# Optimization experiments

Hardware: AMD Instinct MI355X
Metric: run time of the kernel (lower is better)

Reference implementation:

```python
import jax, jax.numpy as jnp
import numpy as np

N_NODES = 100000
N_EDGES = 1600000
IN_FEATS, HID, NUM_CLS = 128, 128, 40


def setup_inputs() -> dict:
    key = jax.random.key(0)
    ks = jax.random.split(key, 5)
    x = jax.random.normal(ks[0], (N_NODES, IN_FEATS), dtype=jnp.float32)
    # xavier-like scale for weights
    W1 = jax.random.normal(ks[1], (IN_FEATS, HID), dtype=jnp.float32) * (1.0 / np.sqrt(IN_FEATS))
    b1 = jnp.zeros((HID,), dtype=jnp.float32)
    W2 = jax.random.normal(ks[2], (HID, NUM_CLS), dtype=jnp.float32) * (1.0 / np.sqrt(HID))
    b2 = jnp.zeros((NUM_CLS,), dtype=jnp.float32)
    src = jax.random.randint(ks[3], (N_EDGES,), 0, N_NODES, dtype=jnp.int32)
    dst = jax.random.randint(ks[4], (N_EDGES,), 0, N_NODES, dtype=jnp.int32)
    return {"x": x, "W1": W1, "b1": b1, "W2": W2, "b2": b2, "src": src, "dst": dst}


def _graph_conv(h, W, b, src, dst, src_norm, dst_norm, n_nodes):
    # DGL GraphConv, norm='both': D_out^{-1/2} A D_in^{-1/2} H W + b
    # (weight-first vs aggregate-first ordering in DGL is mathematically identical)
    hs = h * src_norm[:, None]                      # [N, d] source-side norm
    msg = hs[src]                                   # [E, d] gather
    agg = jax.ops.segment_sum(msg, dst, num_segments=n_nodes)  # [N, d] scatter-add
    agg = agg * dst_norm[:, None]                   # dest-side norm
    return agg @ W + b


def reference(x, W1, b1, W2, b2, src, dst):
    n = x.shape[0]
    ones = jnp.ones(src.shape[0], dtype=x.dtype)
    out_deg = jnp.clip(jax.ops.segment_sum(ones, src, num_segments=n), 1.0)
    in_deg = jnp.clip(jax.ops.segment_sum(ones, dst, num_segments=n), 1.0)
    src_norm = out_deg ** -0.5
    dst_norm = in_deg ** -0.5
    h = jax.nn.relu(_graph_conv(x, W1, b1, src, dst, src_norm, dst_norm, n))
    return _graph_conv(h, W2, b2, src, dst, src_norm, dst_norm, n)
```

## Files before the change

### kernel.cpp

```cpp
#include <hip/hip_runtime.h>

constexpr int NN   = 100000;
constexpr int NE   = 1600000;
constexpr int INF  = 128;
constexpr int NC   = 40;

constexpr int BKSH = 9;
constexpr int NBK  = (NN + 511) / 512;
constexpr int EPB  = 4096;
constexpr int PBLK = (NE + EPB - 1) / EPB;
constexpr int CAP  = 14336;
constexpr int HB   = 391;

typedef __attribute__((ext_vector_type(8))) short short8;
typedef __attribute__((ext_vector_type(4))) float f32x4;

__device__ __forceinline__ float bflo(unsigned int u) { return __uint_as_float(u << 16); }
__device__ __forceinline__ float bfhi(unsigned int u) { return __uint_as_float(u & 0xffff0000u); }
__device__ __forceinline__ unsigned short f2bf(float f) {
    unsigned int u = __float_as_uint(f);
    return (unsigned short)((u + 0x7fffu + ((u >> 16) & 1u)) >> 16);
}
__device__ __forceinline__ unsigned int pack2(float a, float b) {
    return (unsigned int)f2bf(a) | ((unsigned int)f2bf(b) << 16);
}

__global__ __launch_bounds__(256) void histconv_kernel(const int* __restrict__ src,
                                                       const int* __restrict__ dst,
                                                       unsigned int* __restrict__ bcntD,
                                                       unsigned int* __restrict__ bcntS,
                                                       const float* __restrict__ x,
                                                       const float* __restrict__ W1,
                                                       const float* __restrict__ W2,
                                                       unsigned short* __restrict__ xh,
                                                       unsigned short* __restrict__ w1t,
                                                       unsigned short* __restrict__ w2t) {
    const int b = blockIdx.x;
    const int tid = threadIdx.x;
    if (b < HB) {
        __shared__ unsigned int hcD[NBK];
        __shared__ unsigned int hcS[NBK];
        for (int i = tid; i < NBK; i += 256) { hcD[i] = 0u; hcS[i] = 0u; }
        __syncthreads();
        int gid = b * 256 + tid;
        int stride = HB * 256;
        for (int e = gid; e < NE; e += stride) {
            atomicAdd(&hcD[dst[e] >> BKSH], 1u);
            atomicAdd(&hcS[src[e] >> BKSH], 1u);
        }
        __syncthreads();
        for (int i = tid; i < NBK; i += 256) {
            if (hcD[i]) atomicAdd(&bcntD[i], hcD[i]);
            if (hcS[i]) atomicAdd(&bcntS[i], hcS[i]);
        }
    } else if (b < HB + 6250) {
        int j = (b - HB) * 256 + tid;
        float4 v0 = ((const float4*)x)[2 * j];
        float4 v1 = ((const float4*)x)[2 * j + 1];
        uint4 o;
        o.x = pack2(v0.x, v0.y);
        o.y = pack2(v0.z, v0.w);
        o.z = pack2(v1.x, v1.y);
        o.w = pack2(v1.z, v1.w);
        ((uint4*)xh)[j] = o;
    } else if (b == HB + 6250) {
        for (int i = tid; i < 128 * 128; i += 256) {
            int k = i >> 7, n = i & 127;
            w1t[n * 128 + k] = f2bf(W1[i]);
        }
    } else {
        for (int i = tid; i < 48 * 128; i += 256) {
            int n = i >> 7, k = i & 127;
            w2t[i] = f2bf((n < NC) ? W2[k * NC + n] : 0.f);
        }
    }
}

__global__ __launch_bounds__(256) void partition_kernel(const int* __restrict__ src,
                                                        const int* __restrict__ dst,
                                                        const unsigned int* __restrict__ bcntD,
                                                        const unsigned int* __restrict__ bcntS,
                                                        int* __restrict__ curD_g,
                                                        int* __restrict__ curS_g,
                                                        int* __restrict__ epartsD,
                                                        unsigned short* __restrict__ epartsS) {
    __shared__ int sc[256];
    __shared__ int cntD[NBK], gadjD[NBK], curD[NBK];
    __shared__ int cntS[NBK], gadjS[NBK], curS[NBK];
    __shared__ int baselD[NBK], baselS[NBK];
    __shared__ int stageD[EPB];
    __shared__ unsigned short stageS[EPB];
    __shared__ unsigned char bidD[EPB];
    __shared__ unsigned char bidS[EPB];
    const int tid = threadIdx.x;
    const int e0 = blockIdx.x * EPB;
    const int total = min(EPB, NE - e0);

    {
        int v = (tid < NBK) ? (int)bcntD[tid] : 0;
        sc[tid] = v;
        __syncthreads();
        for (int off = 1; off < 256; off <<= 1) {
            int t = (tid >= off) ? sc[tid - off] : 0;
            __syncthreads();
            sc[tid] += t;
            __syncthreads();
        }
        if (tid < NBK) baselD[tid] = sc[tid] - v;
        __syncthreads();
        v = (tid < NBK) ? (int)bcntS[tid] : 0;
        sc[tid] = v;
        __syncthreads();
        for (int off = 1; off < 256; off <<= 1) {
            int t = (tid >= off) ? sc[tid - off] : 0;
            __syncthreads();
            sc[tid] += t;
            __syncthreads();
        }
        if (tid < NBK) baselS[tid] = sc[tid] - v;
    }
    for (int i = tid; i < NBK; i += 256) { cntD[i] = 0; cntS[i] = 0; }
    __syncthreads();
    for (int i = tid; i < total; i += 256) {
        atomicAdd(&cntD[dst[e0 + i] >> BKSH], 1);
        atomicAdd(&cntS[src[e0 + i] >> BKSH], 1);
    }
    __syncthreads();
    {
        int v = (tid < NBK) ? cntD[tid] : 0;
        sc[tid] = v;
        __syncthreads();
        for (int off = 1; off < 256; off <<= 1) {
            int t = (tid >= off) ? sc[tid - off] : 0;
            __syncthreads();
            sc[tid] += t;
            __syncthreads();
        }
        if (tid < NBK) {
            int excl = sc[tid] - v;
            curD[tid] = excl;
            int g = (v > 0) ? atomicAdd(&curD_g[tid], v) : 0;
            gadjD[tid] = baselD[tid] + g - excl;
        }
        __syncthreads();
        v = (tid < NBK) ? cntS[tid] : 0;
        sc[tid] = v;
        __syncthreads();
        for (int off = 1; off < 256; off <<= 1) {
            int t = (tid >= off) ? sc[tid - off] : 0;
            __syncthreads();
            sc[tid] += t;
            __syncthreads();
        }
        if (tid < NBK) {
            int excl = sc[tid] - v;
            curS[tid] = excl;
            int g = (v > 0) ? atomicAdd(&curS_g[tid], v) : 0;
            gadjS[tid] = baselS[tid] + g - excl;
        }
    }
    __syncthreads();
    for (int i = tid; i < total; i += 256) {
        int s = src[e0 + i];
        int d = dst[e0 + i];
        int bD = d >> BKSH;
        int offD = atomicAdd(&curD[bD], 1);
        stageD[offD] = s | ((d - (bD << BKSH)) << 17);
        bidD[offD] = (unsigned char)bD;
        int bS = s >> BKSH;
        int offS = atomicAdd(&curS[bS], 1);
        stageS[offS] = (unsigned short)(s - (bS << BKSH));
        bidS[offS] = (unsigned char)bS;
    }
    __syncthreads();
    for (int j = tid; j < total; j += 256) {
        int b = bidD[j];
        epartsD[gadjD[b] + j] = stageD[j];
    }
    for (int j = tid; j < total; j += 256) {
        int b = bidS[j];
        epartsS[gadjS[b] + j] = stageS[j];
    }
}

__global__ __launch_bounds__(512) void pass2_kernel(const int* __restrict__ epartsD,
                                                    const unsigned short* __restrict__ epartsS,
                                                    const unsigned int* __restrict__ bcntD,
                                                    const unsigned int* __restrict__ bcntS,
                                                    int* __restrict__ row_ptr,
                                                    int* __restrict__ esrc,
                                                    float* __restrict__ srcn,
                                                    float* __restrict__ dstn) {
    __shared__ int hist[512];
    __shared__ int cur[512];
    __shared__ int histS[512];
    __shared__ int lesrc[CAP];
    __shared__ int base_s, cnt_s, baseS_s, cntS_s;
    const int tid = threadIdx.x;
    const int b = blockIdx.x;

    {
        int v = (tid < NBK) ? (int)bcntD[tid] : 0;
        hist[tid] = v;
        __syncthreads();
        for (int off = 1; off < 512; off <<= 1) {
            int t = (tid >= off) ? hist[tid - off] : 0;
            __syncthreads();
            hist[tid] += t;
            __syncthreads();
        }
        if (tid == b) { base_s = hist[b] - v; cnt_s = v; }
        __syncthreads();
        v = (tid < NBK) ? (int)bcntS[tid] : 0;
        hist[tid] = v;
        __syncthreads();
        for (int off = 1; off < 512; off <<= 1) {
            int t = (tid >= off) ? hist[tid - off] : 0;
            __syncthreads();
            hist[tid] += t;
            __syncthreads();
        }
        if (tid == b) { baseS_s = hist[b] - v; cntS_s = v; }
        __syncthreads();
    }
    const int base = base_s;
    const int cnt = cnt_s;
    const int baseS = baseS_s;
    const int cntS = cntS_s;
    const int n0 = b << BKSH;
    const int nloc = min(512, NN - n0);

    hist[tid] = 0;
    histS[tid] = 0;
    __syncthreads();
    for (int j = tid; j < cnt; j += 512)
        atomicAdd(&hist[epartsD[base + j] >> 17], 1);
    for (int j = tid; j < cntS; j += 512)
        atomicAdd(&histS[(int)epartsS[baseS + j]], 1);
    __syncthreads();
    int myc = hist[tid];
    int mycS = histS[tid];
    for (int off = 1; off < 512; off <<= 1) {
        int t = (tid >= off) ? hist[tid - off] : 0;
        __syncthreads();
        hist[tid] += t;
        __syncthreads();
    }
    int excl = hist[tid] - myc;
    cur[tid] = excl;
    if (tid < nloc) {
        int g = n0 + tid;
        row_ptr[g] = base + excl;
        dstn[g] = rsqrtf(fmaxf((float)myc, 1.0f));
        srcn[g] = rsqrtf(fmaxf((float)mycS, 1.0f));
    }
    if (b == NBK - 1 && tid == 0) row_ptr[NN] = NE;
    __syncthreads();
    if (cnt <= CAP) {
        for (int j = tid; j < cnt; j += 512) {
            int rec = epartsD[base + j];
            int pos = atomicAdd(&cur[rec >> 17], 1);
            lesrc[pos] = rec & 0x1FFFF;
        }
        __syncthreads();
        for (int j = tid; j < cnt; j += 512) esrc[base + j] = lesrc[j];
    } else {
        for (int j = tid; j < cnt; j += 512) {
            int rec = epartsD[base + j];
            int pos = atomicAdd(&cur[rec >> 17], 1);
            esrc[base + pos] = rec & 0x1FFFF;
        }
    }
}

__global__ __launch_bounds__(256) void gather1_kernel(const int* __restrict__ row_ptr,
                                                      const int* __restrict__ esrc,
                                                      const unsigned short* __restrict__ xh,
                                                      const float* __restrict__ src_norm,
                                                      unsigned short* __restrict__ aggb) {
    int node = (blockIdx.x * blockDim.x + threadIdx.x) >> 6;
    int lane = threadIdx.x & 63;
    if (node >= NN) return;
    int beg = __builtin_amdgcn_readfirstlane(row_ptr[node]);
    int end = __builtin_amdgcn_readfirstlane(row_ptr[node + 1]);
    const int quad = lane >> 4;
    const int l16  = lane & 15;
    float acc0 = 0.f, acc1 = 0.f, acc2 = 0.f, acc3 = 0.f;
    float acc4 = 0.f, acc5 = 0.f, acc6 = 0.f, acc7 = 0.f;
    for (int e = beg; e < end; e += 16) {
        const int rem = end - e;
        int s[4];
#pragma unroll
        for (int t = 0; t < 4; ++t) {
            int slot = t * 4 + quad;
            int idx = (slot < rem) ? (e + slot) : beg;
            s[t] = esrc[idx];
        }
        float n[4];
        uint4 u[4];
#pragma unroll
        for (int t = 0; t < 4; ++t) {
            int slot = t * 4 + quad;
            n[t] = (slot < rem) ? src_norm[s[t]] : 0.f;
            u[t] = ((const uint4*)(xh + (size_t)s[t] * INF))[l16];
        }
#pragma unroll
        for (int t = 0; t < 4; ++t) {
            acc0 += bflo(u[t].x) * n[t];
            acc1 += bfhi(u[t].x) * n[t];
            acc2 += bflo(u[t].y) * n[t];
            acc3 += bfhi(u[t].y) * n[t];
            acc4 += bflo(u[t].z) * n[t];
            acc5 += bfhi(u[t].z) * n[t];
            acc6 += bflo(u[t].w) * n[t];
            acc7 += bfhi(u[t].w) * n[t];
        }
    }
    acc0 += __shfl_down(acc0, 32); acc1 += __shfl_down(acc1, 32);
    acc2 += __shfl_down(acc2, 32); acc3 += __shfl_down(acc3, 32);
    acc4 += __shfl_down(acc4, 32); acc5 += __shfl_down(acc5, 32);
    acc6 += __shfl_down(acc6, 32); acc7 += __shfl_down(acc7, 32);
    acc0 += __shfl_down(acc0, 16); acc1 += __shfl_down(acc1, 16);
    acc2 += __shfl_down(acc2, 16); acc3 += __shfl_down(acc3, 16);
    acc4 += __shfl_down(acc4, 16); acc5 += __shfl_down(acc5, 16);
    acc6 += __shfl_down(acc6, 16); acc7 += __shfl_down(acc7, 16);
    if (lane < 16) {
        uint4 o;
        o.x = pack2(acc0, acc1);
        o.y = pack2(acc2, acc3);
        o.z = pack2(acc4, acc5);
        o.w = pack2(acc6, acc7);
        ((uint4*)(aggb + (size_t)node * INF))[l16] = o;
    }
}

__global__ __launch_bounds__(256) void gemm12_kernel(const unsigned short* __restrict__ aggb,
                                                     const unsigned short* __restrict__ w1t,
                                                     const unsigned short* __restrict__ w2t,
                                                     const float* __restrict__ b1,
                                                     const float* __restrict__ dstn,
                                                     const float* __restrict__ srcn,
                                                     unsigned short* __restrict__ hwb) {
    __shared__ unsigned short At[64 * 128];
    __shared__ unsigned short W1l[128 * 128];
    __shared__ unsigned short W2l[48 * 128];
    __shared__ float dn[64], sn[64], b1l[128];
    const int tid = threadIdx.x;
    const int r0 = blockIdx.x * 64;

    {
        const uint4* g1 = (const uint4*)w1t;
        uint4* s1 = (uint4*)W1l;
        for (int i = tid; i < 2048; i += 256) s1[i] = g1[i];
        const uint4* g2 = (const uint4*)w2t;
        uint4* s2 = (uint4*)W2l;
        for (int i = tid; i < 768; i += 256) s2[i] = g2[i];
    }
    {
        const uint4* g = (const uint4*)(aggb + (size_t)r0 * 128);
        uint4* s = (uint4*)At;
        for (int i = tid; i < 1024; i += 256) {
            int row = i >> 4;
            uint4 v = make_uint4(0, 0, 0, 0);
            if (r0 + row < NN) v = g[i];
            s[i] = v;
        }
    }
    if (tid < 64) {
        int r = r0 + tid;
        dn[tid] = (r < NN) ? dstn[r] : 0.f;
        sn[tid] = (r < NN) ? srcn[r] : 0.f;
    }
    if (tid >= 64 && tid < 192) b1l[tid - 64] = b1[tid - 64];
    __syncthreads();

    const int wv    = tid >> 6;
    const int lane  = tid & 63;
    const int lrow  = lane & 15;
    const int lquad = lane >> 4;

    short8 afrag[4];
#pragma unroll
    for (int ks = 0; ks < 4; ++ks)
        afrag[ks] = *(const short8*)&At[(wv * 16 + lrow) * 128 + ks * 32 + lquad * 8];
    float hreg[8][4];
#pragma unroll
    for (int nt = 0; nt < 8; ++nt) {
        f32x4 acc = {0.f, 0.f, 0.f, 0.f};
#pragma unroll
        for (int ks = 0; ks < 4; ++ks) {
            short8 bfr = *(const short8*)&W1l[(nt * 16 + lrow) * 128 + ks * 32 + lquad * 8];
            acc = __builtin_amdgcn_mfma_f32_16x16x32_bf16(afrag[ks], bfr, acc, 0, 0, 0);
        }
#pragma unroll
        for (int i = 0; i < 4; ++i) hreg[nt][i] = acc[i];
    }
#pragma unroll
    for (int nt = 0; nt < 8; ++nt) {
        int col = nt * 16 + lrow;
        float bb = b1l[col];
#pragma unroll
        for (int i = 0; i < 4; ++i) {
            int row = wv * 16 + lquad * 4 + i;
            At[row * 128 + col] = f2bf(fmaxf(hreg[nt][i] * dn[row] + bb, 0.f));
        }
    }
    __syncthreads();

#pragma unroll
    for (int ks = 0; ks < 4; ++ks)
        afrag[ks] = *(const short8*)&At[(wv * 16 + lrow) * 128 + ks * 32 + lquad * 8];
#pragma unroll
    for (int nt = 0; nt < 3; ++nt) {
        f32x4 acc = {0.f, 0.f, 0.f, 0.f};
#pragma unroll
        for (int ks = 0; ks < 4; ++ks) {
            short8 bfr = *(const short8*)&W2l[(nt * 16 + lrow) * 128 + ks * 32 + lquad * 8];
            acc = __builtin_amdgcn_mfma_f32_16x16x32_bf16(afrag[ks], bfr, acc, 0, 0, 0);
        }
        int col = nt * 16 + lrow;
        if (col < NC) {
#pragma unroll
            for (int i = 0; i < 4; ++i) {
                int row = wv * 16 + lquad * 4 + i;
                int grow = r0 + row;
                if (grow < NN)
                    hwb[(size_t)grow * NC + col] = f2bf(acc[i] * sn[row]);
            }
        }
    }
}

__global__ __launch_bounds__(256) void gather2_kernel(const int* __restrict__ row_ptr,
                                                      const int* __restrict__ esrc,
                                                      const unsigned short* __restrict__ hwb,
                                                      const float* __restrict__ dst_norm,
                                                      const float* __restrict__ b2,
                                                      float* __restrict__ out) {
    int node = (blockIdx.x * blockDim.x + threadIdx.x) >> 6;
    int lane = threadIdx.x & 63;
    if (node >= NN) return;
    int beg = __builtin_amdgcn_readfirstlane(row_ptr[node]);
    int end = __builtin_amdgcn_readfirstlane(row_ptr[node + 1]);
    const int g = lane / 10;
    const int j = lane - g * 10;
    const bool active = (g < 6);
    float4 acc = make_float4(0.f, 0.f, 0.f, 0.f);
    for (int e = beg; e < end; e += 18) {
        const int rem = end - e;
        int s[3];
        float m[3];
#pragma unroll
        for (int q = 0; q < 3; ++q) {
            int slot = q * 6 + g;
            bool v = active && (slot < rem);
            int idx = v ? (e + slot) : beg;
            s[q] = esrc[idx];
            m[q] = v ? 1.f : 0.f;
        }
        uint2 u[3];
#pragma unroll
        for (int q = 0; q < 3; ++q)
            u[q] = ((const uint2*)(hwb + (size_t)s[q] * NC))[j];
#pragma unroll
        for (int q = 0; q < 3; ++q) {
            acc.x += bflo(u[q].x) * m[q];
            acc.y += bfhi(u[q].x) * m[q];
            acc.z += bflo(u[q].y) * m[q];
            acc.w += bfhi(u[q].y) * m[q];
        }
    }
    float4 tot = acc;
#pragma unroll
    for (int k = 1; k < 6; ++k) {
        tot.x += __shfl(acc.x, j + 10 * k);
        tot.y += __shfl(acc.y, j + 10 * k);
        tot.z += __shfl(acc.z, j + 10 * k);
        tot.w += __shfl(acc.w, j + 10 * k);
    }
    if (lane < 10) {
        float dnv = dst_norm[node];
        float4 bb = ((const float4*)b2)[j];
        float4 o;
        o.x = tot.x * dnv + bb.x;
        o.y = tot.y * dnv + bb.y;
        o.z = tot.z * dnv + bb.z;
        o.w = tot.w * dnv + bb.w;
        ((float4*)(out + (size_t)node * NC))[j] = o;
    }
}

extern "C" void kernel_launch(void* const* d_in, const int* in_sizes, int n_in,
                              void* d_out, int out_size, void* d_ws, size_t ws_size,
                              hipStream_t stream) {
    const float* x   = (const float*)d_in[0];
    const float* W1  = (const float*)d_in[1];
    const float* b1  = (const float*)d_in[2];
    const float* W2  = (const float*)d_in[3];
    const float* b2  = (const float*)d_in[4];
    const int*   src = (const int*)d_in[5];
    const int*   dst = (const int*)d_in[6];
    float* out = (float*)d_out;

    float* srcn = (float*)d_ws;
    unsigned int* bcntD = (unsigned int*)(srcn + NN);
    unsigned int* bcntS = bcntD + 256;
    int* curD = (int*)(bcntS + 256);
    int* curS = curD + 256;
    int* row_ptr = curS + 256;
    float* dstn  = (float*)(row_ptr + NN + 1);
    int* esrc    = (int*)(dstn + NN);
    size_t ofs = (size_t)NN + 1024 + (NN + 1) + NN + NE;
    ofs = (ofs + 3) & ~(size_t)3;
    unsigned short* aggb = (unsigned short*)((float*)d_ws + ofs);
    unsigned short* xh   = aggb + (size_t)NN * INF;
    unsigned short* w1t  = xh + (size_t)NN * INF;
    unsigned short* w2t  = w1t + 128 * 128;
    unsigned short* hwb  = xh;

    int* epartsD = (int*)d_out;
    unsigned short* epartsS = (unsigned short*)(epartsD + NE);

    hipMemsetAsync(bcntD, 0, 1024 * sizeof(int), stream);

    histconv_kernel<<<HB + 6252, 256, 0, stream>>>(src, dst, bcntD, bcntS,
                                                   x, W1, W2, xh, w1t, w2t);
    partition_kernel<<<PBLK, 256, 0, stream>>>(src, dst, bcntD, bcntS, curD, curS,
                                               epartsD, epartsS);
    pass2_kernel<<<NBK, 512, 0, stream>>>(epartsD, epartsS, bcntD, bcntS,
                                          row_ptr, esrc, srcn, dstn);
    gather1_kernel<<<(NN * 64 + 255) / 256, 256, 0, stream>>>(row_ptr, esrc, xh,
                                                              srcn, aggb);
    gemm12_kernel<<<(NN + 63) / 64, 256, 0, stream>>>(aggb, w1t, w2t, b1, dstn,
                                                      srcn, hwb);
    gather2_kernel<<<(NN * 64 + 255) / 256, 256, 0, stream>>>(row_ptr, esrc, hwb,
                                                              dstn, b2, out);
}
```

Baseline: 321.0 us.

## Fuse layer-1 gather into GEMM kernel, aggregating rows directly into LDS

Merges the first neighbor-gather kernel into the two-layer GEMM kernel: each wave aggregates 16 nodes serially into the shared A tile, then runs the MFMA GEMMs. This removes the bf16 aggb round trip through global memory and one launch. Weight tiles are now read straight from global memory instead of being staged in LDS, and the gather unroll goes from 16 to 24 edges. The risk is much lower gather parallelism, since one wave handles 16 nodes one after another. The __syncthreads before reading the hidden tile for the second GEMM was removed, which relies on each wave touching only its own 16 rows.

After: 318.7 us. About the same (-0.7%).

```diff
diff --git a/kernel.cpp b/kernel.cpp
--- a/kernel.cpp
+++ b/kernel.cpp
@@ -273,99 +273,22 @@
     }
 }
 
-__global__ __launch_bounds__(256) void gather1_kernel(const int* __restrict__ row_ptr,
-                                                      const int* __restrict__ esrc,
-                                                      const unsigned short* __restrict__ xh,
-                                                      const float* __restrict__ src_norm,
-                                                      unsigned short* __restrict__ aggb) {
-    int node = (blockIdx.x * blockDim.x + threadIdx.x) >> 6;
-    int lane = threadIdx.x & 63;
-    if (node >= NN) return;
-    int beg = __builtin_amdgcn_readfirstlane(row_ptr[node]);
-    int end = __builtin_amdgcn_readfirstlane(row_ptr[node + 1]);
-    const int quad = lane >> 4;
-    const int l16  = lane & 15;
-    float acc0 = 0.f, acc1 = 0.f, acc2 = 0.f, acc3 = 0.f;
-    float acc4 = 0.f, acc5 = 0.f, acc6 = 0.f, acc7 = 0.f;
-    for (int e = beg; e < end; e += 16) {
-        const int rem = end - e;
-        int s[4];
-#pragma unroll
-        for (int t = 0; t < 4; ++t) {
-            int slot = t * 4 + quad;
-            int idx = (slot < rem) ? (e + slot) : beg;
-            s[t] = esrc[idx];
-        }
-        float n[4];
-        uint4 u[4];
-#pragma unroll
-        for (int t = 0; t < 4; ++t) {
-            int slot = t * 4 + quad;
-            n[t] = (slot < rem) ? src_norm[s[t]] : 0.f;
-            u[t] = ((const uint4*)(xh + (size_t)s[t] * INF))[l16];
-        }
-#pragma unroll
-        for (int t = 0; t < 4; ++t) {
-            acc0 += bflo(u[t].x) * n[t];
-            acc1 += bfhi(u[t].x) * n[t];
-            acc2 += bflo(u[t].y) * n[t];
-            acc3 += bfhi(u[t].y) * n[t];
-            acc4 += bflo(u[t].z) * n[t];
-            acc5 += bfhi(u[t].z) * n[t];
-            acc6 += bflo(u[t].w) * n[t];
-            acc7 += bfhi(u[t].w) * n[t];
-        }
-    }
-    acc0 += __shfl_down(acc0, 32); acc1 += __shfl_down(acc1, 32);
-    acc2 += __shfl_down(acc2, 32); acc3 += __shfl_down(acc3, 32);
-    acc4 += __shfl_down(acc4, 32); acc5 += __shfl_down(acc5, 32);
-    acc6 += __shfl_down(acc6, 32); acc7 += __shfl_down(acc7, 32);
-    acc0 += __shfl_down(acc0, 16); acc1 += __shfl_down(acc1, 16);
-    acc2 += __shfl_down(acc2, 16); acc3 += __shfl_down(acc3, 16);
-    acc4 += __shfl_down(acc4, 16); acc5 += __shfl_down(acc5, 16);
-    acc6 += __shfl_down(acc6, 16); acc7 += __shfl_down(acc7, 16);
-    if (lane < 16) {
-        uint4 o;
-        o.x = pack2(acc0, acc1);
-        o.y = pack2(acc2, acc3);
-        o.z = pack2(acc4, acc5);
-        o.w = pack2(acc6, acc7);
-        ((uint4*)(aggb + (size_t)node * INF))[l16] = o;
-    }
-}
-
-__global__ __launch_bounds__(256) void gemm12_kernel(const unsigned short* __restrict__ aggb,
-                                                     const unsigned short* __restrict__ w1t,
-                                                     const unsigned short* __restrict__ w2t,
-                                                     const float* __restrict__ b1,
-                                                     const float* __restrict__ dstn,
-                                                     const float* __restrict__ srcn,
-                                                     unsigned short* __restrict__ hwb) {
+__global__ __launch_bounds__(256) void fused_kernel(const int* __restrict__ row_ptr,
+                                                    const int* __restrict__ esrc,
+                                                    const unsigned short* __restrict__ xh,
+                                                    const float* __restrict__ srcn,
+                                                    const unsigned short* __restrict__ w1t,
+                                                    const unsigned short* __restrict__ w2t,
+                                                    const float* __restrict__ b1,
+                                                    const float* __restrict__ dstn,
+                                                    unsigned short* __restrict__ hwb) {
     __shared__ unsigned short At[64 * 128];
-    __shared__ unsigned short W1l[128 * 128];
-    __shared__ unsigned short W2l[48 * 128];
     __shared__ float dn[64], sn[64], b1l[128];
-    const int tid = threadIdx.x;
-    const int r0 = blockIdx.x * 64;
-
-    {
-        const uint4* g1 = (const uint4*)w1t;
-        uint4* s1 = (uint4*)W1l;
-        for (int i = tid; i < 2048; i += 256) s1[i] = g1[i];
-        const uint4* g2 = (const uint4*)w2t;
-        uint4* s2 = (uint4*)W2l;
-        for (int i = tid; i < 768; i += 256) s2[i] = g2[i];
-    }
-    {
-        const uint4* g = (const uint4*)(aggb + (size_t)r0 * 128);
-        uint4* s = (uint4*)At;
-        for (int i = tid; i < 1024; i += 256) {
-            int row = i >> 4;
-            uint4 v = make_uint4(0, 0, 0, 0);
-            if (r0 + row < NN) v = g[i];
-            s[i] = v;
-        }
-    }
+    const int tid  = threadIdx.x;
+    const int r0   = blockIdx.x * 64;
+    const int wv   = tid >> 6;
+    const int lane = tid & 63;
+
     if (tid < 64) {
         int r = r0 + tid;
         dn[tid] = (r < NN) ? dstn[r] : 0.f;
@@ -374,8 +297,62 @@
     if (tid >= 64 && tid < 192) b1l[tid - 64] = b1[tid - 64];
     __syncthreads();
 
-    const int wv    = tid >> 6;
-    const int lane  = tid & 63;
+    const int quad = lane >> 4;
+    const int l16  = lane & 15;
+    for (int i = 0; i < 16; ++i) {
+        const int node = r0 + wv * 16 + i;
+        float a0 = 0.f, a1 = 0.f, a2 = 0.f, a3 = 0.f;
+        float a4 = 0.f, a5 = 0.f, a6 = 0.f, a7 = 0.f;
+        if (node < NN) {
+            int beg = __builtin_amdgcn_readfirstlane(row_ptr[node]);
+            int end = __builtin_amdgcn_readfirstlane(row_ptr[node + 1]);
+            for (int e = beg; e < end; e += 24) {
+                const int rem = end - e;
+                int s[6];
+#pragma unroll
+                for (int t = 0; t < 6; ++t) {
+                    int slot = t * 4 + quad;
+                    s[t] = esrc[(slot < rem) ? (e + slot) : beg];
+                }
+                float n[6];
+                uint4 u[6];
+#pragma unroll
+                for (int t = 0; t < 6; ++t) {
+                    int slot = t * 4 + quad;
+                    n[t] = (slot < rem) ? srcn[s[t]] : 0.f;
+                    u[t] = ((const uint4*)(xh + (size_t)s[t] * INF))[l16];
+                }
+#pragma unroll
+                for (int t = 0; t < 6; ++t) {
+                    a0 += bflo(u[t].x) * n[t];
+                    a1 += bfhi(u[t].x) * n[t];
+                    a2 += bflo(u[t].y) * n[t];
+                    a3 += bfhi(u[t].y) * n[t];
+                    a4 += bflo(u[t].z) * n[t];
+                    a5 += bfhi(u[t].z) * n[t];
+                    a6 += bflo(u[t].w) * n[t];
+                    a7 += bfhi(u[t].w) * n[t];
+                }
+            }
+        }
+        a0 += __shfl_down(a0, 32); a1 += __shfl_down(a1, 32);
+        a2 += __shfl_down(a2, 32); a3 += __shfl_down(a3, 32);
+        a4 += __shfl_down(a4, 32); a5 += __shfl_down(a5, 32);
+        a6 += __shfl_down(a6, 32); a7 += __shfl_down(a7, 32);
+        a0 += __shfl_down(a0, 16); a1 += __shfl_down(a1, 16);
+        a2 += __shfl_down(a2, 16); a3 += __shfl_down(a3, 16);
+        a4 += __shfl_down(a4, 16); a5 += __shfl_down(a5, 16);
+        a6 += __shfl_down(a6, 16); a7 += __shfl_down(a7, 16);
+        if (lane < 16) {
+            uint4 o;
+            o.x = pack2(a0, a1);
+            o.y = pack2(a2, a3);
+            o.z = pack2(a4, a5);
+            o.w = pack2(a6, a7);
+            *(uint4*)&At[(wv * 16 + i) * 128 + l16 * 8] = o;
+        }
+    }
+
     const int lrow  = lane & 15;
     const int lquad = lane >> 4;
 
@@ -389,7 +366,7 @@
         f32x4 acc = {0.f, 0.f, 0.f, 0.f};
 #pragma unroll
         for (int ks = 0; ks < 4; ++ks) {
-            short8 bfr = *(const short8*)&W1l[(nt * 16 + lrow) * 128 + ks * 32 + lquad * 8];
+            short8 bfr = *(const short8*)&w1t[(nt * 16 + lrow) * 128 + ks * 32 + lquad * 8];
             acc = __builtin_amdgcn_mfma_f32_16x16x32_bf16(afrag[ks], bfr, acc, 0, 0, 0);
         }
 #pragma unroll
@@ -405,7 +382,6 @@
             At[row * 128 + col] = f2bf(fmaxf(hreg[nt][i] * dn[row] + bb, 0.f));
         }
     }
-    __syncthreads();
 
 #pragma unroll
     for (int ks = 0; ks < 4; ++ks)
@@ -415,7 +391,7 @@
         f32x4 acc = {0.f, 0.f, 0.f, 0.f};
 #pragma unroll
         for (int ks = 0; ks < 4; ++ks) {
-            short8 bfr = *(const short8*)&W2l[(nt * 16 + lrow) * 128 + ks * 32 + lquad * 8];
+            short8 bfr = *(const short8*)&w2t[(nt * 16 + lrow) * 128 + ks * 32 + lquad * 8];
             acc = __builtin_amdgcn_mfma_f32_16x16x32_bf16(afrag[ks], bfr, acc, 0, 0, 0);
         }
         int col = nt * 16 + lrow;
@@ -512,11 +488,10 @@
     int* esrc    = (int*)(dstn + NN);
     size_t ofs = (size_t)NN + 1024 + (NN + 1) + NN + NE;
     ofs = (ofs + 3) & ~(size_t)3;
-    unsigned short* aggb = (unsigned short*)((float*)d_ws + ofs);
-    unsigned short* xh   = aggb + (size_t)NN * INF;
+    unsigned short* xh   = (unsigned short*)((float*)d_ws + ofs);
     unsigned short* w1t  = xh + (size_t)NN * INF;
     unsigned short* w2t  = w1t + 128 * 128;
-    unsigned short* hwb  = xh;
+    unsigned short* hwb  = w2t + 48 * 128;
 
     int* epartsD = (int*)d_out;
     unsigned short* epartsS = (unsigned short*)(epartsD + NE);
@@ -529,10 +504,8 @@
                                                epartsD, epartsS);
     pass2_kernel<<<NBK, 512, 0, stream>>>(epartsD, epartsS, bcntD, bcntS,
                                           row_ptr, esrc, srcn, dstn);
-    gather1_kernel<<<(NN * 64 + 255) / 256, 256, 0, stream>>>(row_ptr, esrc, xh,
-                                                              srcn, aggb);
-    gemm12_kernel<<<(NN + 63) / 64, 256, 0, stream>>>(aggb, w1t, w2t, b1, dstn,
-                                                      srcn, hwb);
+    fused_kernel<<<(NN + 63) / 64, 256, 0, stream>>>(row_ptr, esrc, xh, srcn,
+                                                     w1t, w2t, b1, dstn, hwb);
     gather2_kernel<<<(NN * 64 + 255) / 256, 256, 0, stream>>>(row_ptr, esrc, hwb,
                                                               dstn, b2, out);
 }
```

## Halve bucket size, hoist bucket-base scan, and shrink GEMM tile with global weight reads

Applied to the files above, without the earlier changes.

Bucket width drops from 512 to 256 nodes, so pass2 runs twice as many smaller blocks (256 threads, smaller shared staging) and the partition kernel uses 512 threads. The per-block prefix scan over the global bucket counts moves into a single basescan kernel, removing redundant scans from every partition and pass2 block. The fused GEMM now processes 32 rows per block and reads weight fragments straight from global memory instead of staging W1/W2 in LDS, cutting shared memory to raise occupancy. The layer-2 GEMM then runs on only half the waves, and hwb gets its own buffer instead of aliasing xh. The cost is an extra launch and more uncached-in-LDS weight traffic.

New measurement: 322.6 us. No clear change (+0.5%).

```diff
diff --git a/kernel.cpp b/kernel.cpp
--- a/kernel.cpp
+++ b/kernel.cpp
@@ -5,11 +5,11 @@
 constexpr int INF  = 128;
 constexpr int NC   = 40;
 
-constexpr int BKSH = 9;
-constexpr int NBK  = (NN + 511) / 512;
+constexpr int BKSH = 8;
+constexpr int NBK  = (NN + 255) / 256;
 constexpr int EPB  = 4096;
 constexpr int PBLK = (NE + EPB - 1) / EPB;
-constexpr int CAP  = 14336;
+constexpr int CAP  = 8192;
 constexpr int HB   = 391;
 
 typedef __attribute__((ext_vector_type(8))) short short8;
@@ -76,171 +76,153 @@
     }
 }
 
-__global__ __launch_bounds__(256) void partition_kernel(const int* __restrict__ src,
+__global__ __launch_bounds__(512) void basescan_kernel(const unsigned int* __restrict__ bcntD,
+                                                       const unsigned int* __restrict__ bcntS,
+                                                       int* __restrict__ baseD,
+                                                       int* __restrict__ baseS) {
+    __shared__ int sc[512];
+    const int tid = threadIdx.x;
+    int v = (tid < NBK) ? (int)bcntD[tid] : 0;
+    sc[tid] = v;
+    __syncthreads();
+    for (int off = 1; off < 512; off <<= 1) {
+        int t = (tid >= off) ? sc[tid - off] : 0;
+        __syncthreads();
+        sc[tid] += t;
+        __syncthreads();
+    }
+    if (tid < NBK) baseD[tid] = sc[tid] - v;
+    __syncthreads();
+    v = (tid < NBK) ? (int)bcntS[tid] : 0;
+    sc[tid] = v;
+    __syncthreads();
+    for (int off = 1; off < 512; off <<= 1) {
+        int t = (tid >= off) ? sc[tid - off] : 0;
+        __syncthreads();
+        sc[tid] += t;
+        __syncthreads();
+    }
+    if (tid < NBK) baseS[tid] = sc[tid] - v;
+}
+
+__global__ __launch_bounds__(512) void partition_kernel(const int* __restrict__ src,
                                                         const int* __restrict__ dst,
-                                                        const unsigned int* __restrict__ bcntD,
-                                                        const unsigned int* __restrict__ bcntS,
+                                                        const int* __restrict__ baseD,
+                                                        const int* __restrict__ baseS,
                                                         int* __restrict__ curD_g,
                                                         int* __restrict__ curS_g,
                                                         int* __restrict__ epartsD,
                                                         unsigned short* __restrict__ epartsS) {
-    __shared__ int sc[256];
+    __shared__ int sc[512];
     __shared__ int cntD[NBK], gadjD[NBK], curD[NBK];
     __shared__ int cntS[NBK], gadjS[NBK], curS[NBK];
-    __shared__ int baselD[NBK], baselS[NBK];
     __shared__ int stageD[EPB];
     __shared__ unsigned short stageS[EPB];
-    __shared__ unsigned char bidD[EPB];
-    __shared__ unsigned char bidS[EPB];
+    __shared__ unsigned short bidD[EPB];
+    __shared__ unsigned short bidS[EPB];
     const int tid = threadIdx.x;
     const int e0 = blockIdx.x * EPB;
     const int total = min(EPB, NE - e0);
 
+    for (int i = tid; i < NBK; i += 512) { cntD[i] = 0; cntS[i] = 0; }
+    __syncthreads();
+    for (int i = tid; i < total; i += 512) {
+        atomicAdd(&cntD[dst[e0 + i] >> BKSH], 1);
+        atomicAdd(&cntS[src[e0 + i] >> BKSH], 1);
+    }
+    __syncthreads();
     {
-        int v = (tid < NBK) ? (int)bcntD[tid] : 0;
+        int v = (tid < NBK) ? cntD[tid] : 0;
         sc[tid] = v;
         __syncthreads();
-        for (int off = 1; off < 256; off <<= 1) {
+        for (int off = 1; off < 512; off <<= 1) {
             int t = (tid >= off) ? sc[tid - off] : 0;
             __syncthreads();
             sc[tid] += t;
             __syncthreads();
         }
-        if (tid < NBK) baselD[tid] = sc[tid] - v;
-        __syncthreads();
-        v = (tid < NBK) ? (int)bcntS[tid] : 0;
+        if (tid < NBK) {
+            int excl = sc[tid] - v;
+            curD[tid] = excl;
+            int g = (v > 0) ? atomicAdd(&curD_g[tid], v) : 0;
+            gadjD[tid] = baseD[tid] + g - excl;
+        }
+        __syncthreads();
+        v = (tid < NBK) ? cntS[tid] : 0;
         sc[tid] = v;
         __syncthreads();
-        for (int off = 1; off < 256; off <<= 1) {
+        for (int off = 1; off < 512; off <<= 1) {
             int t = (tid >= off) ? sc[tid - off] : 0;
             __syncthreads();
             sc[tid] += t;
             __syncthreads();
         }
-        if (tid < NBK) baselS[tid] = sc[tid] - v;
-    }
-    for (int i = tid; i < NBK; i += 256) { cntD[i] = 0; cntS[i] = 0; }
-    __syncthreads();
-    for (int i = tid; i < total; i += 256) {
-        atomicAdd(&cntD[dst[e0 + i] >> BKSH], 1);
-        atomicAdd(&cntS[src[e0 + i] >> BKSH], 1);
-    }
-    __syncthreads();
-    {
-        int v = (tid < NBK) ? cntD[tid] : 0;
-        sc[tid] = v;
-        __syncthreads();
-        for (int off = 1; off < 256; off <<= 1) {
-            int t = (tid >= off) ? sc[tid - off] : 0;
-            __syncthreads();
-            sc[tid] += t;
-            __syncthreads();
-        }
-        if (tid < NBK) {
-            int excl = sc[tid] - v;
-            curD[tid] = excl;
-            int g = (v > 0) ? atomicAdd(&curD_g[tid], v) : 0;
-            gadjD[tid] = baselD[tid] + g - excl;
-        }
-        __syncthreads();
-        v = (tid < NBK) ? cntS[tid] : 0;
-        sc[tid] = v;
-        __syncthreads();
-        for (int off = 1; off < 256; off <<= 1) {
-            int t = (tid >= off) ? sc[tid - off] : 0;
-            __syncthreads();
-            sc[tid] += t;
-            __syncthreads();
-        }
         if (tid < NBK) {
             int excl = sc[tid] - v;
             curS[tid] = excl;
             int g = (v > 0) ? atomicAdd(&curS_g[tid], v) : 0;
-            gadjS[tid] = baselS[tid] + g - excl;
-        }
-    }
-    __syncthreads();
-    for (int i = tid; i < total; i += 256) {
+            gadjS[tid] = baseS[tid] + g - excl;
+        }
+    }
+    __syncthreads();
+    for (int i = tid; i < total; i += 512) {
         int s = src[e0 + i];
         int d = dst[e0 + i];
         int bD = d >> BKSH;
         int offD = atomicAdd(&curD[bD], 1);
         stageD[offD] = s | ((d - (bD << BKSH)) << 17);
-        bidD[offD] = (unsigned char)bD;
+        bidD[offD] = (unsigned short)bD;
         int bS = s >> BKSH;
         int offS = atomicAdd(&curS[bS], 1);
         stageS[offS] = (unsigned short)(s - (bS << BKSH));
-        bidS[offS] = (unsigned char)bS;
-    }
-    __syncthreads();
-    for (int j = tid; j < total; j += 256) {
+        bidS[offS] = (unsigned short)bS;
+    }
+    __syncthreads();
+    for (int j = tid; j < total; j += 512) {
         int b = bidD[j];
         epartsD[gadjD[b] + j] = stageD[j];
     }
-    for (int j = tid; j < total; j += 256) {
+    for (int j = tid; j < total; j += 512) {
         int b = bidS[j];
         epartsS[gadjS[b] + j] = stageS[j];
     }
 }
 
-__global__ __launch_bounds__(512) void pass2_kernel(const int* __restrict__ epartsD,
+__global__ __launch_bounds__(256) void pass2_kernel(const int* __restrict__ epartsD,
                                                     const unsigned short* __restrict__ epartsS,
+                                                    const int* __restrict__ baseD,
+                                                    const int* __restrict__ baseS_g,
                                                     const unsigned int* __restrict__ bcntD,
                                                     const unsigned int* __restrict__ bcntS,
                                                     int* __restrict__ row_ptr,
                                                     int* __restrict__ esrc,
                                                     float* __restrict__ srcn,
                                                     float* __restrict__ dstn) {
-    __shared__ int hist[512];
-    __shared__ int cur[512];
-    __shared__ int histS[512];
+    __shared__ int hist[256];
+    __shared__ int cur[256];
+    __shared__ int histS[256];
     __shared__ int lesrc[CAP];
-    __shared__ int base_s, cnt_s, baseS_s, cntS_s;
     const int tid = threadIdx.x;
     const int b = blockIdx.x;
 
-    {
-        int v = (tid < NBK) ? (int)bcntD[tid] : 0;
-        hist[tid] = v;
-        __syncthreads();
-        for (int off = 1; off < 512; off <<= 1) {
-            int t = (tid >= off) ? hist[tid - off] : 0;
-            __syncthreads();
-            hist[tid] += t;
-            __syncthreads();
-        }
-        if (tid == b) { base_s = hist[b] - v; cnt_s = v; }
-        __syncthreads();
-        v = (tid < NBK) ? (int)bcntS[tid] : 0;
-        hist[tid] = v;
-        __syncthreads();
-        for (int off = 1; off < 512; off <<= 1) {
-            int t = (tid >= off) ? hist[tid - off] : 0;
-            __syncthreads();
-            hist[tid] += t;
-            __syncthreads();
-        }
-        if (tid == b) { baseS_s = hist[b] - v; cntS_s = v; }
-        __syncthreads();
-    }
-    const int base = base_s;
-    const int cnt = cnt_s;
-    const int baseS = baseS_s;
-    const int cntS = cntS_s;
+    const int base  = baseD[b];
+    const int cnt   = (int)bcntD[b];
+    const int baseS = baseS_g[b];
+    const int cntS  = (int)bcntS[b];
     const int n0 = b << BKSH;
-    const int nloc = min(512, NN - n0);
+    const int nloc = min(256, NN - n0);
 
     hist[tid] = 0;
     histS[tid] = 0;
     __syncthreads();
-    for (int j = tid; j < cnt; j += 512)
+    for (int j = tid; j < cnt; j += 256)
         atomicAdd(&hist[epartsD[base + j] >> 17], 1);
-    for (int j = tid; j < cntS; j += 512)
+    for (int j = tid; j < cntS; j += 256)
         atomicAdd(&histS[(int)epartsS[baseS + j]], 1);
     __syncthreads();
     int myc = hist[tid];
     int mycS = histS[tid];
-    for (int off = 1; off < 512; off <<= 1) {
+    for (int off = 1; off < 256; off <<= 1) {
         int t = (tid >= off) ? hist[tid - off] : 0;
         __syncthreads();
         hist[tid] += t;
@@ -257,15 +239,15 @@
     if (b == NBK - 1 && tid == 0) row_ptr[NN] = NE;
     __syncthreads();
     if (cnt <= CAP) {
-        for (int j = tid; j < cnt; j += 512) {
+        for (int j = tid; j < cnt; j += 256) {
             int rec = epartsD[base + j];
             int pos = atomicAdd(&cur[rec >> 17], 1);
             lesrc[pos] = rec & 0x1FFFF;
         }
         __syncthreads();
-        for (int j = tid; j < cnt; j += 512) esrc[base + j] = lesrc[j];
+        for (int j = tid; j < cnt; j += 256) esrc[base + j] = lesrc[j];
     } else {
-        for (int j = tid; j < cnt; j += 512) {
+        for (int j = tid; j < cnt; j += 256) {
             int rec = epartsD[base + j];
             int pos = atomicAdd(&cur[rec >> 17], 1);
             esrc[base + pos] = rec & 0x1FFFF;
@@ -334,39 +316,31 @@
     }
 }
 
-__global__ __launch_bounds__(256) void gemm12_kernel(const unsigned short* __restrict__ aggb,
-                                                     const unsigned short* __restrict__ w1t,
-                                                     const unsigned short* __restrict__ w2t,
-                                                     const float* __restrict__ b1,
-                                                     const float* __restrict__ dstn,
-                                                     const float* __restrict__ srcn,
-                                                     unsigned short* __restrict__ hwb) {
-    __shared__ unsigned short At[64 * 128];
-    __shared__ unsigned short W1l[128 * 128];
-    __shared__ unsigned short W2l[48 * 128];
-    __shared__ float dn[64], sn[64], b1l[128];
-    const int tid = threadIdx.x;
-    const int r0 = blockIdx.x * 64;
-
-    {
-        const uint4* g1 = (const uint4*)w1t;
-        uint4* s1 = (uint4*)W1l;
-        for (int i = tid; i < 2048; i += 256) s1[i] = g1[i];
-        const uint4* g2 = (const uint4*)w2t;
-        uint4* s2 = (uint4*)W2l;
-        for (int i = tid; i < 768; i += 256) s2[i] = g2[i];
-    }
+__global__ __launch_bounds__(256, 4) void gemm12_kernel(const unsigned short* __restrict__ aggb,
+                                                        const unsigned short* __restrict__ w1t,
+                                                        const unsigned short* __restrict__ w2t,
+                                                        const float* __restrict__ b1,
+                                                        const float* __restrict__ dstn,
+                                                        const float* __restrict__ srcn,
+                                                        unsigned short* __restrict__ hwb) {
+    __shared__ unsigned short At[32 * 128];
+    __shared__ float dn[32], sn[32], b1l[128];
+    const int tid  = threadIdx.x;
+    const int r0   = blockIdx.x * 32;
+    const int wv   = tid >> 6;
+    const int lane = tid & 63;
+
     {
         const uint4* g = (const uint4*)(aggb + (size_t)r0 * 128);
         uint4* s = (uint4*)At;
-        for (int i = tid; i < 1024; i += 256) {
+        for (int i = tid; i < 512; i += 256) {
             int row = i >> 4;
             uint4 v = make_uint4(0, 0, 0, 0);
             if (r0 + row < NN) v = g[i];
             s[i] = v;
         }
     }
-    if (tid < 64) {
+    if (tid < 32) {
         int r = r0 + tid;
         dn[tid] = (r < NN) ? dstn[r] : 0.f;
         sn[tid] = (r < NN) ? srcn[r] : 0.f;
@@ -374,58 +348,63 @@
     if (tid >= 64 && tid < 192) b1l[tid - 64] = b1[tid - 64];
     __syncthreads();
 
-    const int wv    = tid >> 6;
-    const int lane  = tid & 63;
     const int lrow  = lane & 15;
     const int lquad = lane >> 4;
+    const int rt    = wv >> 1;
+    const int ntB   = (wv & 1) * 4;
 
     short8 afrag[4];
 #pragma unroll
     for (int ks = 0; ks < 4; ++ks)
-        afrag[ks] = *(const short8*)&At[(wv * 16 + lrow) * 128 + ks * 32 + lquad * 8];
-    float hreg[8][4];
-#pragma unroll
-    for (int nt = 0; nt < 8; ++nt) {
+        afrag[ks] = *(const short8*)&At[(rt * 16 + lrow) * 128 + ks * 32 + lquad * 8];
+    __syncthreads();
+
+    float hreg[4][4];
+#pragma unroll
+    for (int nt2 = 0; nt2 < 4; ++nt2) {
         f32x4 acc = {0.f, 0.f, 0.f, 0.f};
 #pragma unroll
         for (int ks = 0; ks < 4; ++ks) {
-            short8 bfr = *(const short8*)&W1l[(nt * 16 + lrow) * 128 + ks * 32 + lquad * 8];
+            short8 bfr = *(const short8*)&w1t[((ntB + nt2) * 16 + lrow) * 128 + ks * 32 + lquad * 8];
             acc = __builtin_amdgcn_mfma_f32_16x16x32_bf16(afrag[ks], bfr, acc, 0, 0, 0);
         }
 #pragma unroll
-        for (int i = 0; i < 4; ++i) hreg[nt][i] = acc[i];
-    }
-#pragma unroll
-    for (int nt = 0; nt < 8; ++nt) {
-        int col = nt * 16 + lrow;
+        for (int i = 0; i < 4; ++i) hreg[nt2][i] = acc[i];
+    }
+#pragma unroll
+    for (int nt2 = 0; nt2 < 4; ++nt2) {
+        int col = (ntB + nt2) * 16 + lrow;
         float bb = b1l[col];
 #pragma unroll
         for (int i = 0; i < 4; ++i) {
-            int row = wv * 16 + lquad * 4 + i;
-            At[row * 128 + col] = f2bf(fmaxf(hreg[nt][i] * dn[row] + bb, 0.f));
-        }
-    }
-    __syncthreads();
-
-#pragma unroll
-    for (int ks = 0; ks < 4; ++ks)
-        afrag[ks] = *(const short8*)&At[(wv * 16 + lrow) * 128 + ks * 32 + lquad * 8];
-#pragma unroll
-    for (int nt = 0; nt < 3; ++nt) {
-        f32x4 acc = {0.f, 0.f, 0.f, 0.f};
-#pragma unroll
-        for (int ks = 0; ks < 4; ++ks) {
-            short8 bfr = *(const short8*)&W2l[(nt * 16 + lrow) * 128 + ks * 32 + lquad * 8];
-            acc = __builtin_amdgcn_mfma_f32_16x16x32_bf16(afrag[ks], bfr, acc, 0, 0, 0);
-        }
-        int col = nt * 16 + lrow;
-        if (col < NC) {
-#pragma unroll
-            for (int i = 0; i < 4; ++i) {
-                int row = wv * 16 + lquad * 4 + i;
-                int grow = r0 + row;
-                if (grow < NN)
-                    hwb[(size_t)grow * NC + col] = f2bf(acc[i] * sn[row]);
+            int row = rt * 16 + lquad * 4 + i;
+            At[row * 128 + col] = f2bf(fmaxf(hreg[nt2][i] * dn[row] + bb, 0.f));
+        }
+    }
+    __syncthreads();
+
+    if ((wv & 1) == 0) {
+        short8 hf[4];
+#pragma unroll
+        for (int ks = 0; ks < 4; ++ks)
+            hf[ks] = *(const short8*)&At[(rt * 16 + lrow) * 128 + ks * 32 + lquad * 8];
+#pragma unroll
+        for (int nt = 0; nt < 3; ++nt) {
+            f32x4 acc = {0.f, 0.f, 0.f, 0.f};
+#pragma unroll
+            for (int ks = 0; ks < 4; ++ks) {
+                short8 bfr = *(const short8*)&w2t[(nt * 16 + lrow) * 128 + ks * 32 + lquad * 8];
+                acc = __builtin_amdgcn_mfma_f32_16x16x32_bf16(hf[ks], bfr, acc, 0, 0, 0);
+            }
+            int col = nt * 16 + lrow;
+            if (col < NC) {
+#pragma unroll
+                for (int i = 0; i < 4; ++i) {
+                    int row = rt * 16 + lquad * 4 + i;
+                    int grow = r0 + row;
+                    if (grow < NN)
+                        hwb[(size_t)grow * NC + col] = f2bf(acc[i] * sn[row]);
+                }
             }
         }
     }
@@ -504,34 +483,37 @@
 
     float* srcn = (float*)d_ws;
     unsigned int* bcntD = (unsigned int*)(srcn + NN);
-    unsigned int* bcntS = bcntD + 256;
-    int* curD = (int*)(bcntS + 256);
-    int* curS = curD + 256;
-    int* row_ptr = curS + 256;
+    unsigned int* bcntS = bcntD + 512;
+    int* curDg = (int*)(bcntS + 512);
+    int* curSg = curDg + 512;
+    int* baseD = curSg + 512;
+    int* baseS = baseD + 512;
+    int* row_ptr = baseS + 512;
     float* dstn  = (float*)(row_ptr + NN + 1);
     int* esrc    = (int*)(dstn + NN);
-    size_t ofs = (size_t)NN + 1024 + (NN + 1) + NN + NE;
+    size_t ofs = (size_t)NN + 3072 + (NN + 1) + NN + NE;
     ofs = (ofs + 3) & ~(size_t)3;
     unsigned short* aggb = (unsigned short*)((float*)d_ws + ofs);
     unsigned short* xh   = aggb + (size_t)NN * INF;
     unsigned short* w1t  = xh + (size_t)NN * INF;
     unsigned short* w2t  = w1t + 128 * 128;
-    unsigned short* hwb  = xh;
+    unsigned short* hwb  = w2t + 48 * 128;
 
     int* epartsD = (int*)d_out;
     unsigned short* epartsS = (unsigned short*)(epartsD + NE);
 
-    hipMemsetAsync(bcntD, 0, 1024 * sizeof(int), stream);
+    hipMemsetAsync(bcntD, 0, 2048 * sizeof(int), stream);
 
     histconv_kernel<<<HB + 6252, 256, 0, stream>>>(src, dst, bcntD, bcntS,
                                                    x, W1, W2, xh, w1t, w2t);
-    partition_kernel<<<PBLK, 256, 0, stream>>>(src, dst, bcntD, bcntS, curD, curS,
+    basescan_kernel<<<1, 512, 0, stream>>>(bcntD, bcntS, baseD, baseS);
+    partition_kernel<<<PBLK, 512, 0, stream>>>(src, dst, baseD, baseS, curDg, curSg,
                                                epartsD, epartsS);
-    pass2_kernel<<<NBK, 512, 0, stream>>>(epartsD, epartsS, bcntD, bcntS,
-                                          row_ptr, esrc, srcn, dstn);
+    pass2_kernel<<<NBK, 256, 0, stream>>>(epartsD, epartsS, baseD, baseS,
+                                          bcntD, bcntS, row_ptr, esrc, srcn, dstn);
     gather1_kernel<<<(NN * 64 + 255) / 256, 256, 0, stream>>>(row_ptr, esrc, xh,
                                                               srcn, aggb);
-    gemm12_kernel<<<(NN + 63) / 64, 256, 0, stream>>>(aggb, w1t, w2t, b1, dstn,
+    gemm12_kernel<<<(NN + 31) / 32, 256, 0, stream>>>(aggb, w1t, w2t, b1, dstn,
                                                       srcn, hwb);
     gather2_kernel<<<(NN * 64 + 255) / 256, 256, 0, stream>>>(row_ptr, esrc, hwb,
                                                               dstn, b2, out);
```
